# Kernel tuning notes

Measured on AMD Instinct MI355X. Metric: run time of the kernel, lower is better.

Reference implementation:

```python
import jax, jax.numpy as jnp
import numpy as np

jax.config.update("jax_enable_x64", True)

B, N, M_EQ, D_INEQ = 64, 128, 32, 64
RHO = 1.0
THRES = 1e-5
MAX_ITERS = 5000  # safety cap (original loops until relative objective change <= 1e-5)


def setup_inputs() -> dict:
    key = jax.random.key(0)
    kL, kq, kG, kA, kx0, ks = jax.random.split(key, 6)
    L = jax.random.normal(kL, (B, N, N))
    Q = jnp.einsum('bij,bkj->bik', L, L) / N + jnp.eye(N)  # SPD, well-conditioned
    q = jax.random.normal(kq, (B, N))
    G = jax.random.normal(kG, (B, D_INEQ, N))
    A = jax.random.normal(kA, (B, M_EQ, N))
    x0 = jax.random.normal(kx0, (B, N))
    slack = jax.random.uniform(ks, (B, D_INEQ)) + 0.1
    h = jnp.einsum('bdn,bn->bd', G, x0) + slack  # strictly feasible ineq
    b = jnp.einsum('bmn,bn->bm', A, x0)          # feasible eq
    f32 = jnp.float32
    return {"Q": Q.astype(f32), "q": q.astype(f32), "G": G.astype(f32),
            "h": h.astype(f32), "A": A.astype(f32), "b": b.astype(f32)}


def _alt_diff_batch(Q, q, G, h, A, b):
    """Batched Alt-Diff ADMM QP solve; returns (x [B,n], dx/dq [B,n,n])."""
    Bb, n = q.shape
    d = h.shape[1]
    m = b.shape[1]
    dt = Q.dtype
    AtA = jnp.einsum('bmi,bmj->bij', A, A)
    GtG = jnp.einsum('bdi,bdj->bij', G, G)
    R = -jnp.linalg.inv(Q + RHO * AtA + RHO * GtG)
    ATb = RHO * jnp.einsum('bmn,bm->bn', A, b)
    GTh = RHO * jnp.einsum('bdn,bd->bn', G, h)
    eye = jnp.eye(n, dtype=dt)

    def obj(x):
        return 0.5 * jnp.einsum('bi,bij,bj->b', x, Q, x) + jnp.einsum('bi,bi->b', q, x)

    init = dict(
        xk=jnp.zeros((Bb, n), dt), sk=jnp.zeros((Bb, d), dt),
        lamb=jnp.zeros((Bb, m), dt), nu=jnp.zeros((Bb, d), dt),
        dxk=jnp.zeros((Bb, n, n), dt), dsk=jnp.zeros((Bb, d, n), dt),
        dlamb=jnp.zeros((Bb, m, n), dt), dnu=jnp.zeros((Bb, d, n), dt),
        res_prev=jnp.full((Bb,), 1000.0, dt),   # res = [1000, -100] init
        res_cur=jnp.full((Bb,), -100.0, dt),
        done=jnp.zeros((Bb,), bool),
        it=jnp.zeros((), jnp.int32),
    )

    def cond(s):
        return jnp.logical_and(jnp.any(~s["done"]), s["it"] < MAX_ITERS)

    def body(s):
        xk = jnp.einsum('bij,bj->bi', R,
                        q + jnp.einsum('bmn,bm->bn', A, s["lamb"])
                          + jnp.einsum('bdn,bd->bn', G, s["nu"]) - ATb
                          + RHO * jnp.einsum('bdn,bd->bn', G, s["sk"]) - GTh)
        dxk = jnp.einsum('bij,bjk->bik', R,
                         eye + jnp.einsum('bmn,bmk->bnk', A, s["dlamb"])
                             + jnp.einsum('bdn,bdk->bnk', G, s["dnu"])
                             + RHO * jnp.einsum('bdn,bdk->bnk', G, s["dsk"]))
        Gx = jnp.einsum('bdn,bn->bd', G, xk)
        sk = jax.nn.relu(-(1.0 / RHO) * s["nu"] - (Gx - h))
        sgn = (sk > 0).astype(dt)  # sgn applied to already-relu'd sk, as in source
        dsk = (-1.0 / RHO) * sgn[:, :, None] * (s["dnu"] + RHO * jnp.einsum('bdn,bnk->bdk', G, dxk))
        lamb = s["lamb"] + RHO * (jnp.einsum('bmn,bn->bm', A, xk) - b)
        dlamb = s["dlamb"] + RHO * jnp.einsum('bmn,bnk->bmk', A, dxk)
        nu = s["nu"] + RHO * (Gx + sk - h)
        dnu = s["dnu"] + RHO * (jnp.einsum('bdn,bnk->bdk', G, dxk) + dsk)
        res_new = obj(xk)

        keep = s["done"]

        def sel(old, new):
            mask = keep.reshape((-1,) + (1,) * (new.ndim - 1))
            return jnp.where(mask, old, new)

        res_prev = jnp.where(keep, s["res_prev"], s["res_cur"])
        res_cur = jnp.where(keep, s["res_cur"], res_new)
        done = keep | (jnp.abs((res_cur - res_prev) / res_prev) <= THRES)
        return dict(
            xk=sel(s["xk"], xk), sk=sel(s["sk"], sk),
            lamb=sel(s["lamb"], lamb), nu=sel(s["nu"], nu),
            dxk=sel(s["dxk"], dxk), dsk=sel(s["dsk"], dsk),
            dlamb=sel(s["dlamb"], dlamb), dnu=sel(s["dnu"], dnu),
            res_prev=res_prev, res_cur=res_cur, done=done, it=s["it"] + 1,
        )

    final = jax.lax.while_loop(cond, body, init)
    return final["xk"], final["dxk"]


def reference(Q, q, G, h, A, b):
    out_dtype = q.dtype
    f64 = jnp.float64
    x, _dx = _alt_diff_batch(Q.astype(f64), q.astype(f64), G.astype(f64),
                             h.astype(f64), A.astype(f64), b.astype(f64))
    return x.astype(out_dtype)
```

## Files before the change

### kernel.cpp

```cpp
#include <hip/hip_runtime.h>

#define NN 128
#define ME 32
#define DI 64
#define NZ 96
#define ROWD 130
#define MAXIT 5000

#define OFF_UN 16640
#define ROWB  (OFF_UN)
#define COLB  (OFF_UN + 256)
#define PPK   (OFF_UN)
#define ZEXL  (OFF_UN + 256)
#define ZEXH  (OFF_UN + 384)
#define TVX   (OFF_UN + 448)
#define TV16  (OFF_UN + 576)
#define FLG   (OFF_UN + 608)
#define YBUF  (OFF_UN)
#define KBUF  (OFF_UN + 1536)
#define CPART (OFF_UN + 1024)
#define VP    (OFF_UN + 1280)
#define BASEV (OFF_UN + 1792)
#define QBV   (OFF_UN + 1888)
#define FPART (OFF_UN + 1024)
#define RHSV  (OFF_UN + 1280)
#define XPART (OFF_UN + 1408)
#define CB    (OFF_UN + 2688)
#define QBUF  (OFF_UN + 2816)
#define V1    (OFF_UN + 2944)
#define V2    (OFF_UN + 3072)
#define HB    (OFF_UN + 3200)
#define BB    (OFF_UN + 3264)
#define CST   (OFF_UN + 3296)
#define ZBF   (OFF_UN + 3304)
#define LDS_DBL (OFF_UN + 3400)

typedef __attribute__((ext_vector_type(2))) float f32x2;

__device__ __forceinline__ float rlf(float v, int lane) {
  return __uint_as_float((unsigned)__builtin_amdgcn_readlane((int)__float_as_uint(v), lane));
}
__device__ __forceinline__ f32x2 fma2(f32x2 a, f32x2 b, f32x2 c) {
  return __builtin_elementwise_fma(a, b, c);
}

#define MV2(PA, ZS, L0) {                                                  \
    f32x2 z0 = { rlf(ZS, L0), rlf(ZS, (L0)+1) };                           \
    A0 = fma2(Kp[PA], z0, A0); B0 = fma2(Kp2[PA], z0, B0);                 \
    f32x2 z1 = { rlf(ZS, (L0)+2), rlf(ZS, (L0)+3) };                       \
    A1 = fma2(Kp[(PA)+1], z1, A1); B1 = fma2(Kp2[(PA)+1], z1, B1); }

#define CPY12(LB)                                                          \
  _Pragma("unroll") for (int p = 0; p < 6; ++p) {                          \
    Kp [(LB)+p].x = (float)ldsd[KBUF + (2*p  )*NZ + l];                    \
    Kp [(LB)+p].y = (float)ldsd[KBUF + (2*p+1)*NZ + l];                    \
    Kp2[(LB)+p].x = (float)ldsd[KBUF + (2*p  )*NZ + 64 + lm];              \
    Kp2[(LB)+p].y = (float)ldsd[KBUF + (2*p+1)*NZ + 64 + lm];              \
  }

__global__ __launch_bounds__(256, 1) void altdiff_kernel(
    const float* __restrict__ Qg, const float* __restrict__ qg,
    const float* __restrict__ Gg, const float* __restrict__ hg,
    const float* __restrict__ Ag, const float* __restrict__ bg,
    float* __restrict__ out)
{
  extern __shared__ double ldsd[];

  const int bidx = blockIdx.x;
  const int tid  = threadIdx.x;
  const int w    = tid >> 6;
  const int l    = tid & 63;
  const int lm   = l & 31;
  const int ia   = tid & 127;
  const int hh   = tid >> 7;

  const float* Qb = Qg + (size_t)bidx * NN * NN;
  const float* Ab = Ag + (size_t)bidx * ME * NN;
  const float* Gb = Gg + (size_t)bidx * DI * NN;
  const float* qb = qg + (size_t)bidx * NN;
  const float* hb = hg + (size_t)bidx * DI;
  const float* bv = bg + (size_t)bidx * ME;

  if (tid < DI) ldsd[HB + tid] = (double)hb[tid];
  else if (tid < DI + ME) ldsd[BB + tid - DI] = (double)bv[tid - DI];
  if (tid >= 128) ldsd[QBUF + tid - 128] = (double)qb[tid - 128];

  const int r = tid >> 4, c = tid & 15;
  double acc[8][8];

  {
    const float4* Q4 = (const float4*)Qb;
#pragma unroll
    for (int rr = 0; rr < 8; ++rr) {
      float4 q0 = Q4[((8*r+rr) << 5) + 2*c];
      float4 q1 = Q4[((8*r+rr) << 5) + 2*c + 1];
      acc[rr][0]=(double)q0.x; acc[rr][1]=(double)q0.y; acc[rr][2]=(double)q0.z; acc[rr][3]=(double)q0.w;
      acc[rr][4]=(double)q1.x; acc[rr][5]=(double)q1.y; acc[rr][6]=(double)q1.z; acc[rr][7]=(double)q1.w;
    }
    const float4* A4 = (const float4*)Ab;
    for (int m = 0; m < ME; ++m) {
      float4 u0 = A4[(m << 5) + 2*r], u1 = A4[(m << 5) + 2*r + 1];
      float4 v0 = A4[(m << 5) + 2*c], v1 = A4[(m << 5) + 2*c + 1];
      double uu[8] = {(double)u0.x,(double)u0.y,(double)u0.z,(double)u0.w,
                      (double)u1.x,(double)u1.y,(double)u1.z,(double)u1.w};
      double vv[8] = {(double)v0.x,(double)v0.y,(double)v0.z,(double)v0.w,
                      (double)v1.x,(double)v1.y,(double)v1.z,(double)v1.w};
#pragma unroll
      for (int rr = 0; rr < 8; ++rr)
#pragma unroll
        for (int cc = 0; cc < 8; ++cc)
          acc[rr][cc] = fma(uu[rr], vv[cc], acc[rr][cc]);
    }
    const float4* G4 = (const float4*)Gb;
    for (int d = 0; d < DI; ++d) {
      float4 u0 = G4[(d << 5) + 2*r], u1 = G4[(d << 5) + 2*r + 1];
      float4 v0 = G4[(d << 5) + 2*c], v1 = G4[(d << 5) + 2*c + 1];
      double uu[8] = {(double)u0.x,(double)u0.y,(double)u0.z,(double)u0.w,
                      (double)u1.x,(double)u1.y,(double)u1.z,(double)u1.w};
      double vv[8] = {(double)v0.x,(double)v0.y,(double)v0.z,(double)v0.w,
                      (double)v1.x,(double)v1.y,(double)v1.z,(double)v1.w};
#pragma unroll
      for (int rr = 0; rr < 8; ++rr)
#pragma unroll
        for (int cc = 0; cc < 8; ++cc)
          acc[rr][cc] = fma(uu[rr], vv[cc], acc[rr][cc]);
    }
  }

  {
    if (r == 0) {
#pragma unroll
      for (int cc = 0; cc < 8; ++cc) ldsd[ROWB + 8*c + cc] = acc[0][cc];
    }
    if (c == 0) {
#pragma unroll
      for (int rr = 0; rr < 8; ++rr) ldsd[COLB + 8*r + rr] = acc[rr][0];
    }
    __syncthreads();
    for (int k = 0; k < NN; ++k) {
      const int pb = (k & 1) << 7;
      const int krt = k >> 3, kcl = k & 7;
      double rowk[8], colv[8];
#pragma unroll
      for (int cc = 0; cc < 8; ++cc) rowk[cc] = ldsd[ROWB + pb + 8*c + cc];
#pragma unroll
      for (int rr = 0; rr < 8; ++rr) colv[rr] = ldsd[COLB + pb + 8*r + rr];
      const double dkk  = ldsd[ROWB + pb + k];
      const double rcpd = 1.0 / dkk;
      double rdv[8];
#pragma unroll
      for (int cc = 0; cc < 8; ++cc) rdv[cc] = rowk[cc] * rcpd;
      const bool pivR = (r == krt), pivC = (c == krt);
#pragma unroll
      for (int rr = 0; rr < 8; ++rr) {
        const double cv = colv[rr] * rcpd;
        const bool pr = pivR && (rr == kcl);
#pragma unroll
        for (int cc = 0; cc < 8; ++cc) {
          double gen = fma(-cv, rowk[cc], acc[rr][cc]);
          acc[rr][cc] = pr ? rdv[cc] : gen;
        }
      }
      if (pivC) {
#pragma unroll
        for (int cc = 0; cc < 8; ++cc) if (cc == kcl) {
#pragma unroll
          for (int rr = 0; rr < 8; ++rr) {
            const bool pr2 = pivR && (rr == kcl);
            acc[rr][cc] = pr2 ? -rcpd : colv[rr] * rcpd;
          }
        }
      }
      if (k < NN - 1) {
        const int pb2 = ((k + 1) & 1) << 7;
        const int krt2 = (k + 1) >> 3, kcl2 = (k + 1) & 7;
        if (r == krt2) {
#pragma unroll
          for (int rr = 0; rr < 8; ++rr) if (rr == kcl2) {
#pragma unroll
            for (int cc = 0; cc < 8; ++cc) ldsd[ROWB + pb2 + 8*c + cc] = acc[rr][cc];
          }
        }
        if (c == krt2) {
#pragma unroll
          for (int cc = 0; cc < 8; ++cc) if (cc == kcl2) {
#pragma unroll
            for (int rr = 0; rr < 8; ++rr) ldsd[COLB + pb2 + 8*r + rr] = acc[rr][cc];
          }
        }
      }
      __syncthreads();
    }
#pragma unroll
    for (int rr = 0; rr < 8; ++rr) {
      double2* dst = (double2*)(ldsd + (8*r+rr)*ROWD + 8*c);
#pragma unroll
      for (int t = 0; t < 4; ++t) dst[t] = make_double2(acc[rr][2*t], acc[rr][2*t+1]);
    }
  }
  __syncthreads();

  f32x2 Kp[24], Kp2[24];
  for (int blk = 0; blk < 8; ++blk) {
    {
      const float* gp[6];
#pragma unroll
      for (int jj = 0; jj < 6; ++jj) {
        int it = 12*blk + 6*hh + jj;
        gp[jj] = (it < DI) ? (Gb + it*NN) : (Ab + (it - DI)*NN);
      }
      double a2[6] = {0,0,0,0,0,0};
#pragma unroll 4
      for (int t = 0; t < NN; ++t) {
        double rv = ldsd[t*ROWD + ia];
#pragma unroll
        for (int jj = 0; jj < 6; ++jj)
          a2[jj] = fma(rv, (double)gp[jj][t], a2[jj]);
      }
      double2* yst = (double2*)(ldsd + YBUF + ia*12 + 6*hh);
#pragma unroll
      for (int p = 0; p < 3; ++p) yst[p] = make_double2(a2[2*p], a2[2*p+1]);
    }
    __syncthreads();
    {
      const int r2 = (ia < NZ) ? ia : 0;
      const float* brow = (r2 < DI) ? (Gb + r2*NN) : (Ab + (r2 - DI)*NN);
      double a2[6] = {0,0,0,0,0,0};
#pragma unroll 4
      for (int t = 0; t < NN; ++t) {
        double bvv = (double)brow[t];
        const double2* yr = (const double2*)(ldsd + YBUF + t*12 + 6*hh);
        double2 y0 = yr[0], y1 = yr[1], y2 = yr[2];
        a2[0] = fma(bvv, y0.x, a2[0]); a2[1] = fma(bvv, y0.y, a2[1]);
        a2[2] = fma(bvv, y1.x, a2[2]); a2[3] = fma(bvv, y1.y, a2[3]);
        a2[4] = fma(bvv, y2.x, a2[4]); a2[5] = fma(bvv, y2.y, a2[5]);
      }
      if (ia < NZ) {
#pragma unroll
        for (int jj = 0; jj < 6; ++jj) ldsd[KBUF + (6*hh + jj)*NZ + ia] = a2[jj];
      }
    }
    __syncthreads();
    if (w == 0) {
      if (blk == 0)      { CPY12(0) }
      else if (blk == 1) { CPY12(6) }
      else if (blk == 2) { CPY12(12) }
      else if (blk == 3) { CPY12(18) }
    } else if (w == 1) {
      if (blk == 4)      { CPY12(0) }
      else if (blk == 5) { CPY12(6) }
      else if (blk == 6) { CPY12(12) }
      else if (blk == 7) { CPY12(18) }
    }
    __syncthreads();
  }

  {
    double s = 0;
#pragma unroll 8
    for (int jc = 0; jc < 48; ++jc) {
      int j = 48*hh + jc;
      double coef = (j < DI) ? ldsd[HB + j] : ldsd[BB + j - DI];
      const float* src = (j < DI) ? (Gb + j*NN) : (Ab + (j - DI)*NN);
      s = fma(-(double)src[ia], coef, s);
    }
    ldsd[CPART + hh*128 + ia] = s;
  }
  __syncthreads();
  if (tid < NN) ldsd[CB + tid] = ldsd[QBUF + tid] + ldsd[CPART + tid] + ldsd[CPART + 128 + tid];
  __syncthreads();

  {
    double a = 0, b2 = 0;
#pragma unroll 4
    for (int tt = 0; tt < 64; ++tt) {
      int t = 64*hh + tt;
      double rv = ldsd[t*ROWD + ia];
      a  = fma(rv, ldsd[CB + t], a);
      b2 = fma(rv, ldsd[QBUF + t], b2);
    }
    ldsd[VP + hh*128 + ia] = a;
    ldsd[VP + 256 + hh*128 + ia] = b2;
  }
  __syncthreads();
  if (tid < NN) {
    ldsd[V1 + tid] = ldsd[VP + tid] + ldsd[VP + 128 + tid];
    ldsd[V2 + tid] = ldsd[VP + 256 + tid] + ldsd[VP + 384 + tid];
  }
  __syncthreads();

  {
    const int r2 = (ia < NZ) ? ia : 0;
    const float* brow = (r2 < DI) ? (Gb + r2*NN) : (Ab + (r2 - DI)*NN);
    const int voff = hh ? V2 : V1;
    double s = 0;
#pragma unroll 4
    for (int t = 0; t < NN; ++t) s = fma((double)brow[t], ldsd[voff + t], s);
    if (ia < NZ) ldsd[(hh ? QBV : BASEV) + ia] = s;
  }
  if (w == 0) {
    double pc = ldsd[V1+l]*ldsd[CB+l]   + ldsd[V1+64+l]*ldsd[CB+64+l];
    double pq = ldsd[V1+l]*ldsd[QBUF+l] + ldsd[V1+64+l]*ldsd[QBUF+64+l];
#pragma unroll
    for (int off = 32; off >= 1; off >>= 1) { pc += __shfl_xor(pc, off); pq += __shfl_xor(pq, off); }
    if (l == 0) { ldsd[CST] = pc; ldsd[CST+1] = pq; }
  }
  __syncthreads();

  const double baseA = ldsd[BASEV + l];
  const double baseB = ldsd[BASEV + 64 + lm];
  const double qvA   = ldsd[QBV + l];
  const double qvB   = ldsd[QBV + 64 + lm];
  const double hb2   = ldsd[HB + l] - baseA;
  const double bb2   = baseB - ldsd[BB + lm];
  const double S_uc  = ldsd[CST], S_qu = ldsd[CST + 1];
  double hnb = hb2, lb = bb2;
  double zlo = 0.0, zhi = 0.0;
  double zAlo = 0.0, zAhi = 0.0, zBlo = 0.0, zBhi = 0.0, zClo = 0.0, zChi = 0.0;
  double res_prev = 1000.0, res_cur = -100.0;
  float2 own = make_float2(0.f, 0.f);

  {
    if (w < 2) *(float2*)&ldsd[PPK + w*64 + l] = make_float2(0.f, 0.f);
    if (w == 0) ldsd[ZEXL + 64 + l] = 0.0;
    if (w == 1 && l < 32) ldsd[ZEXH + 32 + l] = 0.0;
    if (tid == 0) { ldsd[FLG] = 0.0; ldsd[FLG + 1] = 0.0; }
  }

  for (int it = 0; it < MAXIT + 3; ++it) {
    __syncthreads();
    const int buf = it & 1, nbuf = buf ^ 1;
    const int bprev = nbuf;
    const double fl = ldsd[FLG + bprev];

    if (w < 2) {
      float2 rem = *(const float2*)&ldsd[PPK + buf*128 + (w ^ 1)*64 + l];
      float slo = own.x + rem.x;
      double t = hnb - (double)slo;
      float zflo = (float)fabs(t);
      float zfhi = 0.f;
      double lamn = 0.0;
      if (w == 1) {
        float shi = own.y + rem.y;
        lamn = lb + (double)shi;
        zfhi = (float)lamn;
      }
      if (it >= 3 && fl != 0.0) break;
      if (w == 0) { zClo = zBlo; zBlo = zAlo; zAlo = zlo; }
      else        { zChi = zBhi; zBhi = zAhi; zAhi = zhi; }
      if (it < MAXIT) {
        if (w == 0) { zlo = fabs(t); ldsd[ZEXL + buf*64 + l] = zlo; }
        hnb = hb2 + fmin(t, 0.0);
        if (w == 1) {
          zhi = lamn; lb = lamn + bb2;
          if (l < 32) ldsd[ZEXH + buf*32 + l] = lamn;
        }
        f32x2 A0 = {0.f, 0.f}, A1 = A0, B0 = A0, B1 = A0;
        if (w == 0) {
          MV2(0,  zflo, 0)  MV2(2,  zflo, 4)  MV2(4,  zflo, 8)  MV2(6,  zflo, 12)
          MV2(8,  zflo, 16) MV2(10, zflo, 20) MV2(12, zflo, 24) MV2(14, zflo, 28)
          MV2(16, zflo, 32) MV2(18, zflo, 36) MV2(20, zflo, 40) MV2(22, zflo, 44)
        } else {
          MV2(0,  zflo, 48) MV2(2,  zflo, 52) MV2(4,  zflo, 56) MV2(6,  zflo, 60)
          MV2(8,  zfhi, 0)  MV2(10, zfhi, 4)  MV2(12, zfhi, 8)  MV2(14, zfhi, 12)
          MV2(16, zfhi, 16) MV2(18, zfhi, 20) MV2(20, zfhi, 24) MV2(22, zfhi, 28)
        }
        f32x2 As = A0 + A1, Bs = B0 + B1;
        float2 np = make_float2(As.x + As.y, Bs.x + Bs.y);
        *(float2*)&ldsd[PPK + nbuf*128 + w*64 + l] = np;
        own = np;
      }
    } else if (w == 2) {
      const float2* pb = (const float2*)(ldsd + PPK + buf*128);
      float2 v0 = pb[l], v1 = pb[64 + l];
      const double zAl = ldsd[ZEXL + bprev*64 + l];
      const double zAh = ldsd[ZEXH + bprev*32 + lm];
      const int g = l & 15;
      const double* tq = ldsd + TVX + bprev*64;
      double a0 = tq[g], a1 = tq[g + 16], a2 = tq[g + 32], a3 = tq[g + 48];
      if (it >= 3 && fl != 0.0) break;
      if (it < MAXIT) {
        float slo_f = v0.x + v1.x;
        float shi_f = v0.y + v1.y;
        double yf  = (double)slo_f + baseA;
        double tvl = fma(qvA, zAl, -0.5*(zAl*(baseA + yf) + yf*yf));
        double yfB = (double)shi_f + baseB;
        double tvh = fma(qvB, zAh, -0.5*(zAh*(baseB + yfB) + yfB*yfB));
        ldsd[TVX + buf*64 + l] = tvl + ((l < 32) ? tvh : 0.0);
      }
      if (l < 16 && it >= 1 && it <= MAXIT)
        ldsd[TV16 + buf*16 + l] = (a0 + a1) + (a2 + a3);
    } else {
      double t1v[16];
      const double2* tp = (const double2*)(ldsd + TV16 + bprev*16);
#pragma unroll
      for (int u = 0; u < 8; ++u) { double2 vv = tp[u]; t1v[2*u] = vv.x; t1v[2*u+1] = vv.y; }
      if (it >= 3 && fl != 0.0) break;
      if (it >= 2 && it <= MAXIT + 1) {
        double s1 = ((t1v[0] + t1v[1]) + (t1v[2] + t1v[3])) + ((t1v[4] + t1v[5]) + (t1v[6] + t1v[7]));
        double s2 = ((t1v[8] + t1v[9]) + (t1v[10] + t1v[11])) + ((t1v[12] + t1v[13]) + (t1v[14] + t1v[15]));
        double obj = (s1 + s2) - 0.5*S_uc + S_qu;
        res_prev = res_cur; res_cur = obj;
        if (l == 0)
          ldsd[FLG + buf] = (fabs(res_cur - res_prev) <= 1e-5 * fabs(res_prev)) ? 1.0 : 0.0;
      }
    }
  }

  if (w == 0) ldsd[ZBF + l] = zClo;
  if (w == 1 && l < 32) ldsd[ZBF + 64 + l] = zChi;
  __syncthreads();
  {
    double s = 0;
#pragma unroll 8
    for (int jc = 0; jc < 48; ++jc) {
      int j = 48*hh + jc;
      double zj = ldsd[ZBF + j];
      const float* src = (j < DI) ? (Gb + j*NN) : (Ab + (j - DI)*NN);
      s = fma((double)src[ia], zj, s);
    }
    ldsd[FPART + hh*128 + ia] = s;
  }
  __syncthreads();
  if (tid < NN) ldsd[RHSV + tid] = ldsd[CB + tid] + ldsd[FPART + tid] + ldsd[FPART + 128 + tid];
  __syncthreads();
  {
    double s = 0;
#pragma unroll 4
    for (int tt = 0; tt < 64; ++tt) {
      int t = 64*hh + tt;
      s = fma(ldsd[t*ROWD + ia], ldsd[RHSV + t], s);
    }
    ldsd[XPART + hh*128 + ia] = s;
  }
  __syncthreads();
  if (tid < NN)
    out[(size_t)bidx * NN + tid] = (float)(ldsd[XPART + tid] + ldsd[XPART + 128 + tid]);
}

extern "C" void kernel_launch(void* const* d_in, const int* in_sizes, int n_in,
                              void* d_out, int out_size, void* d_ws, size_t ws_size,
                              hipStream_t stream) {
  (void)in_sizes; (void)n_in; (void)out_size; (void)d_ws; (void)ws_size;
  const float* Q = (const float*)d_in[0];
  const float* q = (const float*)d_in[1];
  const float* G = (const float*)d_in[2];
  const float* h = (const float*)d_in[3];
  const float* A = (const float*)d_in[4];
  const float* b = (const float*)d_in[5];
  float* out = (float*)d_out;
  const size_t lds_bytes = (size_t)LDS_DBL * sizeof(double);
  altdiff_kernel<<<dim3(64), dim3(256), lds_bytes, stream>>>(Q, q, G, h, A, b, out);
}
```

Before: 631.0 us.

## Split iteration matvec across three wavefronts instead of two

The per-iteration 96x96 matvec over the z vector, previously split across two wavefronts with 48 columns each, is now spread over three wavefronts with 32 columns each. The objective-evaluation and convergence-check wavefronts are merged into one. The aim is to shorten the critical path of each serial ADMM iteration, since each wave does fewer readlane+FMA steps. In exchange, each iteration reads three partial-sum buffers instead of two, and the last wave carries more serial work.

```diff
diff --git a/kernel.cpp b/kernel.cpp
--- a/kernel.cpp
+++ b/kernel.cpp
@@ -11,11 +11,11 @@
 #define ROWB  (OFF_UN)
 #define COLB  (OFF_UN + 256)
 #define PPK   (OFF_UN)
-#define ZEXL  (OFF_UN + 256)
-#define ZEXH  (OFF_UN + 384)
-#define TVX   (OFF_UN + 448)
-#define TV16  (OFF_UN + 576)
-#define FLG   (OFF_UN + 608)
+#define ZEXL  (OFF_UN + 384)
+#define ZEXH  (OFF_UN + 512)
+#define TVX   (OFF_UN + 576)
+#define TV16  (OFF_UN + 704)
+#define FLG   (OFF_UN + 736)
 #define YBUF  (OFF_UN)
 #define KBUF  (OFF_UN + 1536)
 #define CPART (OFF_UN + 1024)
@@ -50,12 +50,13 @@
     f32x2 z1 = { rlf(ZS, (L0)+2), rlf(ZS, (L0)+3) };                       \
     A1 = fma2(Kp[(PA)+1], z1, A1); B1 = fma2(Kp2[(PA)+1], z1, B1); }
 
-#define CPY12(LB)                                                          \
-  _Pragma("unroll") for (int p = 0; p < 6; ++p) {                          \
-    Kp [(LB)+p].x = (float)ldsd[KBUF + (2*p  )*NZ + l];                    \
-    Kp [(LB)+p].y = (float)ldsd[KBUF + (2*p+1)*NZ + l];                    \
-    Kp2[(LB)+p].x = (float)ldsd[KBUF + (2*p  )*NZ + 64 + lm];              \
-    Kp2[(LB)+p].y = (float)ldsd[KBUF + (2*p+1)*NZ + 64 + lm];              \
+#define CPYRANGE(LBASE, KBASE, CNT)                                        \
+  _Pragma("unroll") for (int j = 0; j < (CNT); ++j) {                      \
+    const int lj = (LBASE) + j, kc = (KBASE) + j;                          \
+    float va = (float)ldsd[KBUF + kc*NZ + l];                              \
+    float vb = (float)ldsd[KBUF + kc*NZ + 64 + lm];                        \
+    if ((lj & 1) == 0) { Kp[lj>>1].x = va; Kp2[lj>>1].x = vb; }            \
+    else               { Kp[lj>>1].y = va; Kp2[lj>>1].y = vb; }            \
   }
 
 __global__ __launch_bounds__(256, 1) void altdiff_kernel(
@@ -200,7 +201,7 @@
   }
   __syncthreads();
 
-  f32x2 Kp[24], Kp2[24];
+  f32x2 Kp[16], Kp2[16];
   for (int blk = 0; blk < 8; ++blk) {
     {
       const float* gp[6];
@@ -242,15 +243,18 @@
     }
     __syncthreads();
     if (w == 0) {
-      if (blk == 0)      { CPY12(0) }
-      else if (blk == 1) { CPY12(6) }
-      else if (blk == 2) { CPY12(12) }
-      else if (blk == 3) { CPY12(18) }
+      if (blk == 0)      { CPYRANGE(0,  0, 12) }
+      else if (blk == 1) { CPYRANGE(12, 0, 12) }
+      else if (blk == 2) { CPYRANGE(24, 0, 8) }
     } else if (w == 1) {
-      if (blk == 4)      { CPY12(0) }
-      else if (blk == 5) { CPY12(6) }
-      else if (blk == 6) { CPY12(12) }
-      else if (blk == 7) { CPY12(18) }
+      if (blk == 2)      { CPYRANGE(0,  8, 4) }
+      else if (blk == 3) { CPYRANGE(4,  0, 12) }
+      else if (blk == 4) { CPYRANGE(16, 0, 12) }
+      else if (blk == 5) { CPYRANGE(28, 0, 4) }
+    } else if (w == 2) {
+      if (blk == 5)      { CPYRANGE(0,  4, 8) }
+      else if (blk == 6) { CPYRANGE(8,  0, 12) }
+      else if (blk == 7) { CPYRANGE(20, 0, 12) }
     }
     __syncthreads();
   }
@@ -321,9 +325,9 @@
   float2 own = make_float2(0.f, 0.f);
 
   {
-    if (w < 2) *(float2*)&ldsd[PPK + w*64 + l] = make_float2(0.f, 0.f);
+    if (w < 3) *(float2*)&ldsd[PPK + w*64 + l] = make_float2(0.f, 0.f);
     if (w == 0) ldsd[ZEXL + 64 + l] = 0.0;
-    if (w == 1 && l < 32) ldsd[ZEXH + 32 + l] = 0.0;
+    if (w == 2 && l < 32) ldsd[ZEXH + 32 + l] = 0.0;
     if (tid == 0) { ldsd[FLG] = 0.0; ldsd[FLG + 1] = 0.0; }
   }
 
@@ -332,56 +336,77 @@
     const int buf = it & 1, nbuf = buf ^ 1;
     const int bprev = nbuf;
     const double fl = ldsd[FLG + bprev];
-
-    if (w < 2) {
-      float2 rem = *(const float2*)&ldsd[PPK + buf*128 + (w ^ 1)*64 + l];
-      float slo = own.x + rem.x;
+    const float2* pb = (const float2*)(ldsd + PPK + buf*192);
+
+    if (w == 0) {
+      float2 s1v = pb[64 + l], s2v = pb[128 + l];
+      float slo = (own.x + s1v.x) + s2v.x;
       double t = hnb - (double)slo;
       float zflo = (float)fabs(t);
-      float zfhi = 0.f;
-      double lamn = 0.0;
-      if (w == 1) {
-        float shi = own.y + rem.y;
-        lamn = lb + (double)shi;
-        zfhi = (float)lamn;
-      }
       if (it >= 3 && fl != 0.0) break;
-      if (w == 0) { zClo = zBlo; zBlo = zAlo; zAlo = zlo; }
-      else        { zChi = zBhi; zBhi = zAhi; zAhi = zhi; }
+      zClo = zBlo; zBlo = zAlo; zAlo = zlo;
       if (it < MAXIT) {
-        if (w == 0) { zlo = fabs(t); ldsd[ZEXL + buf*64 + l] = zlo; }
+        zlo = fabs(t);
+        ldsd[ZEXL + buf*64 + l] = zlo;
         hnb = hb2 + fmin(t, 0.0);
-        if (w == 1) {
-          zhi = lamn; lb = lamn + bb2;
-          if (l < 32) ldsd[ZEXH + buf*32 + l] = lamn;
-        }
         f32x2 A0 = {0.f, 0.f}, A1 = A0, B0 = A0, B1 = A0;
-        if (w == 0) {
-          MV2(0,  zflo, 0)  MV2(2,  zflo, 4)  MV2(4,  zflo, 8)  MV2(6,  zflo, 12)
-          MV2(8,  zflo, 16) MV2(10, zflo, 20) MV2(12, zflo, 24) MV2(14, zflo, 28)
-          MV2(16, zflo, 32) MV2(18, zflo, 36) MV2(20, zflo, 40) MV2(22, zflo, 44)
-        } else {
-          MV2(0,  zflo, 48) MV2(2,  zflo, 52) MV2(4,  zflo, 56) MV2(6,  zflo, 60)
-          MV2(8,  zfhi, 0)  MV2(10, zfhi, 4)  MV2(12, zfhi, 8)  MV2(14, zfhi, 12)
-          MV2(16, zfhi, 16) MV2(18, zfhi, 20) MV2(20, zfhi, 24) MV2(22, zfhi, 28)
-        }
+        MV2(0,  zflo, 0)  MV2(2,  zflo, 4)  MV2(4,  zflo, 8)  MV2(6,  zflo, 12)
+        MV2(8,  zflo, 16) MV2(10, zflo, 20) MV2(12, zflo, 24) MV2(14, zflo, 28)
         f32x2 As = A0 + A1, Bs = B0 + B1;
         float2 np = make_float2(As.x + As.y, Bs.x + Bs.y);
-        *(float2*)&ldsd[PPK + nbuf*128 + w*64 + l] = np;
+        *(float2*)&ldsd[PPK + nbuf*192 + l] = np;
         own = np;
       }
+    } else if (w == 1) {
+      float2 s0v = pb[l], s2v = pb[128 + l];
+      float slo = (s0v.x + own.x) + s2v.x;
+      double t = hnb - (double)slo;
+      float zflo = (float)fabs(t);
+      if (it >= 3 && fl != 0.0) break;
+      if (it < MAXIT) {
+        hnb = hb2 + fmin(t, 0.0);
+        f32x2 A0 = {0.f, 0.f}, A1 = A0, B0 = A0, B1 = A0;
+        MV2(0,  zflo, 32) MV2(2,  zflo, 36) MV2(4,  zflo, 40) MV2(6,  zflo, 44)
+        MV2(8,  zflo, 48) MV2(10, zflo, 52) MV2(12, zflo, 56) MV2(14, zflo, 60)
+        f32x2 As = A0 + A1, Bs = B0 + B1;
+        float2 np = make_float2(As.x + As.y, Bs.x + Bs.y);
+        *(float2*)&ldsd[PPK + nbuf*192 + 64 + l] = np;
+        own = np;
+      }
     } else if (w == 2) {
-      const float2* pb = (const float2*)(ldsd + PPK + buf*128);
-      float2 v0 = pb[l], v1 = pb[64 + l];
+      float2 s0v = pb[l], s1v = pb[64 + l];
+      float shi = (s0v.y + s1v.y) + own.y;
+      double lamn = lb + (double)shi;
+      float zfhi = (float)lamn;
+      if (it >= 3 && fl != 0.0) break;
+      zChi = zBhi; zBhi = zAhi; zAhi = zhi;
+      if (it < MAXIT) {
+        zhi = lamn;
+        lb = lamn + bb2;
+        if (l < 32) ldsd[ZEXH + buf*32 + l] = lamn;
+        f32x2 A0 = {0.f, 0.f}, A1 = A0, B0 = A0, B1 = A0;
+        MV2(0,  zfhi, 0)  MV2(2,  zfhi, 4)  MV2(4,  zfhi, 8)  MV2(6,  zfhi, 12)
+        MV2(8,  zfhi, 16) MV2(10, zfhi, 20) MV2(12, zfhi, 24) MV2(14, zfhi, 28)
+        f32x2 As = A0 + A1, Bs = B0 + B1;
+        float2 np = make_float2(As.x + As.y, Bs.x + Bs.y);
+        *(float2*)&ldsd[PPK + nbuf*192 + 128 + l] = np;
+        own = np;
+      }
+    } else {
+      float2 v0 = pb[l], v1 = pb[64 + l], v2 = pb[128 + l];
       const double zAl = ldsd[ZEXL + bprev*64 + l];
       const double zAh = ldsd[ZEXH + bprev*32 + lm];
       const int g = l & 15;
       const double* tq = ldsd + TVX + bprev*64;
       double a0 = tq[g], a1 = tq[g + 16], a2 = tq[g + 32], a3 = tq[g + 48];
+      double t1v[16];
+      const double2* tp = (const double2*)(ldsd + TV16 + bprev*16);
+#pragma unroll
+      for (int u = 0; u < 8; ++u) { double2 vv = tp[u]; t1v[2*u] = vv.x; t1v[2*u+1] = vv.y; }
       if (it >= 3 && fl != 0.0) break;
       if (it < MAXIT) {
-        float slo_f = v0.x + v1.x;
-        float shi_f = v0.y + v1.y;
+        float slo_f = (v0.x + v1.x) + v2.x;
+        float shi_f = (v0.y + v1.y) + v2.y;
         double yf  = (double)slo_f + baseA;
         double tvl = fma(qvA, zAl, -0.5*(zAl*(baseA + yf) + yf*yf));
         double yfB = (double)shi_f + baseB;
@@ -390,12 +415,6 @@
       }
       if (l < 16 && it >= 1 && it <= MAXIT)
         ldsd[TV16 + buf*16 + l] = (a0 + a1) + (a2 + a3);
-    } else {
-      double t1v[16];
-      const double2* tp = (const double2*)(ldsd + TV16 + bprev*16);
-#pragma unroll
-      for (int u = 0; u < 8; ++u) { double2 vv = tp[u]; t1v[2*u] = vv.x; t1v[2*u+1] = vv.y; }
-      if (it >= 3 && fl != 0.0) break;
       if (it >= 2 && it <= MAXIT + 1) {
         double s1 = ((t1v[0] + t1v[1]) + (t1v[2] + t1v[3])) + ((t1v[4] + t1v[5]) + (t1v[6] + t1v[7]));
         double s2 = ((t1v[8] + t1v[9]) + (t1v[10] + t1v[11])) + ((t1v[12] + t1v[13]) + (t1v[14] + t1v[15]));
@@ -408,7 +427,7 @@
   }
 
   if (w == 0) ldsd[ZBF + l] = zClo;
-  if (w == 1 && l < 32) ldsd[ZBF + 64 + l] = zChi;
+  if (w == 2 && l < 32) ldsd[ZBF + 64 + l] = zChi;
   __syncthreads();
   {
     double s = 0;
```

New measurement: 598.7 us (median of 2 runs). -5.1%, faster.

## Split ADMM matvec across all four waves instead of two

Applied to the files above, without the earlier changes.

Spreads the per-iteration 96-wide matvec over four wavefronts, each holding 12 register-resident K columns instead of 24, and has every wave read all four partial-sum buffers from LDS. The objective-term work moves onto wave 2 and the TV16 reduction onto wave 1, so the separate ZEXL/ZEXH exchange buffers go away. The z history is now kept in float rather than double. This should shorten the serial critical path of each iteration and ease register pressure, at the cost of more LDS reads per wave and slightly lower precision in the stored z values.

```diff
diff --git a/kernel.cpp b/kernel.cpp
--- a/kernel.cpp
+++ b/kernel.cpp
@@ -11,11 +11,9 @@
 #define ROWB  (OFF_UN)
 #define COLB  (OFF_UN + 256)
 #define PPK   (OFF_UN)
-#define ZEXL  (OFF_UN + 256)
-#define ZEXH  (OFF_UN + 384)
-#define TVX   (OFF_UN + 448)
-#define TV16  (OFF_UN + 576)
-#define FLG   (OFF_UN + 608)
+#define TVX   (OFF_UN + 512)
+#define TV16  (OFF_UN + 640)
+#define FLG   (OFF_UN + 672)
 #define YBUF  (OFF_UN)
 #define KBUF  (OFF_UN + 1536)
 #define CPART (OFF_UN + 1024)
@@ -200,7 +198,7 @@
   }
   __syncthreads();
 
-  f32x2 Kp[24], Kp2[24];
+  f32x2 Kp[12], Kp2[12];
   for (int blk = 0; blk < 8; ++blk) {
     {
       const float* gp[6];
@@ -241,16 +239,8 @@
       }
     }
     __syncthreads();
-    if (w == 0) {
-      if (blk == 0)      { CPY12(0) }
-      else if (blk == 1) { CPY12(6) }
-      else if (blk == 2) { CPY12(12) }
-      else if (blk == 3) { CPY12(18) }
-    } else if (w == 1) {
-      if (blk == 4)      { CPY12(0) }
-      else if (blk == 5) { CPY12(6) }
-      else if (blk == 6) { CPY12(12) }
-      else if (blk == 7) { CPY12(18) }
+    if (w == (blk >> 1)) {
+      if ((blk & 1) == 0) { CPY12(0) } else { CPY12(6) }
     }
     __syncthreads();
   }
@@ -315,15 +305,15 @@
   const double bb2   = baseB - ldsd[BB + lm];
   const double S_uc  = ldsd[CST], S_qu = ldsd[CST + 1];
   double hnb = hb2, lb = bb2;
-  double zlo = 0.0, zhi = 0.0;
-  double zAlo = 0.0, zAhi = 0.0, zBlo = 0.0, zBhi = 0.0, zClo = 0.0, zChi = 0.0;
+  float hnbf = (float)hnb, lbf = (float)lb;
+  float zpl = 0.f, zph = 0.f;
+  float zpl2 = 0.f, zph2 = 0.f;
+  float zAf_lo = 0.f, zBf_lo = 0.f, zCf_lo = 0.f;
+  float zAf_hi = 0.f, zBf_hi = 0.f, zCf_hi = 0.f;
   double res_prev = 1000.0, res_cur = -100.0;
-  float2 own = make_float2(0.f, 0.f);
-
-  {
-    if (w < 2) *(float2*)&ldsd[PPK + w*64 + l] = make_float2(0.f, 0.f);
-    if (w == 0) ldsd[ZEXL + 64 + l] = 0.0;
-    if (w == 1 && l < 32) ldsd[ZEXH + 32 + l] = 0.0;
+
+  {
+    *(float2*)&ldsd[PPK + w*64 + l] = make_float2(0.f, 0.f);
     if (tid == 0) { ldsd[FLG] = 0.0; ldsd[FLG + 1] = 0.0; }
   }
 
@@ -332,70 +322,82 @@
     const int buf = it & 1, nbuf = buf ^ 1;
     const int bprev = nbuf;
     const double fl = ldsd[FLG + bprev];
-
-    if (w < 2) {
-      float2 rem = *(const float2*)&ldsd[PPK + buf*128 + (w ^ 1)*64 + l];
-      float slo = own.x + rem.x;
-      double t = hnb - (double)slo;
-      float zflo = (float)fabs(t);
-      float zfhi = 0.f;
-      double lamn = 0.0;
-      if (w == 1) {
-        float shi = own.y + rem.y;
-        lamn = lb + (double)shi;
-        zfhi = (float)lamn;
-      }
+    const float2* pb = (const float2*)(ldsd + PPK + buf*256);
+    float2 p0 = pb[l], p1 = pb[64 + l], p2 = pb[128 + l], p3 = pb[192 + l];
+
+    if (w == 0) {
+      float slo = (p0.x + p1.x) + (p2.x + p3.x);
+      float zflo = fabsf(hnbf - slo);
       if (it >= 3 && fl != 0.0) break;
-      if (w == 0) { zClo = zBlo; zBlo = zAlo; zAlo = zlo; }
-      else        { zChi = zBhi; zBhi = zAhi; zAhi = zhi; }
+      zCf_lo = zBf_lo; zBf_lo = zAf_lo; zAf_lo = zpl;
       if (it < MAXIT) {
-        if (w == 0) { zlo = fabs(t); ldsd[ZEXL + buf*64 + l] = zlo; }
-        hnb = hb2 + fmin(t, 0.0);
-        if (w == 1) {
-          zhi = lamn; lb = lamn + bb2;
-          if (l < 32) ldsd[ZEXH + buf*32 + l] = lamn;
-        }
-        f32x2 A0 = {0.f, 0.f}, A1 = A0, B0 = A0, B1 = A0;
-        if (w == 0) {
-          MV2(0,  zflo, 0)  MV2(2,  zflo, 4)  MV2(4,  zflo, 8)  MV2(6,  zflo, 12)
-          MV2(8,  zflo, 16) MV2(10, zflo, 20) MV2(12, zflo, 24) MV2(14, zflo, 28)
-          MV2(16, zflo, 32) MV2(18, zflo, 36) MV2(20, zflo, 40) MV2(22, zflo, 44)
-        } else {
-          MV2(0,  zflo, 48) MV2(2,  zflo, 52) MV2(4,  zflo, 56) MV2(6,  zflo, 60)
-          MV2(8,  zfhi, 0)  MV2(10, zfhi, 4)  MV2(12, zfhi, 8)  MV2(14, zfhi, 12)
-          MV2(16, zfhi, 16) MV2(18, zfhi, 20) MV2(20, zfhi, 24) MV2(22, zfhi, 28)
-        }
+        zpl = zflo;
+        double t = hnb - (double)slo; hnb = hb2 + fmin(t, 0.0); hnbf = (float)hnb;
+        f32x2 A0 = {0.f,0.f}, A1 = A0, B0 = A0, B1 = A0;
+        MV2(0,  zflo, 0)  MV2(2,  zflo, 4)  MV2(4,  zflo, 8)
+        MV2(6,  zflo, 12) MV2(8,  zflo, 16) MV2(10, zflo, 20)
         f32x2 As = A0 + A1, Bs = B0 + B1;
-        float2 np = make_float2(As.x + As.y, Bs.x + Bs.y);
-        *(float2*)&ldsd[PPK + nbuf*128 + w*64 + l] = np;
-        own = np;
-      }
-    } else if (w == 2) {
-      const float2* pb = (const float2*)(ldsd + PPK + buf*128);
-      float2 v0 = pb[l], v1 = pb[64 + l];
-      const double zAl = ldsd[ZEXL + bprev*64 + l];
-      const double zAh = ldsd[ZEXH + bprev*32 + lm];
+        *(float2*)&ldsd[PPK + nbuf*256 + l] = make_float2(As.x + As.y, Bs.x + Bs.y);
+      }
+    } else if (w == 1) {
       const int g = l & 15;
       const double* tq = ldsd + TVX + bprev*64;
       double a0 = tq[g], a1 = tq[g + 16], a2 = tq[g + 32], a3 = tq[g + 48];
+      float slo = (p0.x + p1.x) + (p2.x + p3.x);
+      float zflo = fabsf(hnbf - slo);
       if (it >= 3 && fl != 0.0) break;
       if (it < MAXIT) {
-        float slo_f = v0.x + v1.x;
-        float shi_f = v0.y + v1.y;
-        double yf  = (double)slo_f + baseA;
+        double t = hnb - (double)slo; hnb = hb2 + fmin(t, 0.0); hnbf = (float)hnb;
+        f32x2 A0 = {0.f,0.f}, A1 = A0, B0 = A0, B1 = A0;
+        MV2(0,  zflo, 24) MV2(2,  zflo, 28) MV2(4,  zflo, 32)
+        MV2(6,  zflo, 36) MV2(8,  zflo, 40) MV2(10, zflo, 44)
+        f32x2 As = A0 + A1, Bs = B0 + B1;
+        *(float2*)&ldsd[PPK + nbuf*256 + 64 + l] = make_float2(As.x + As.y, Bs.x + Bs.y);
+      }
+      if (l < 16 && it >= 1 && it <= MAXIT)
+        ldsd[TV16 + buf*16 + l] = (a0 + a1) + (a2 + a3);
+    } else if (w == 2) {
+      float slo = (p0.x + p1.x) + (p2.x + p3.x);
+      float shi = (p0.y + p1.y) + (p2.y + p3.y);
+      float zflo = fabsf(hnbf - slo);
+      float zfhi = lbf + shi;
+      if (it >= 3 && fl != 0.0) break;
+      const float zAl_f = zpl2, zAh_f = zph2;
+      if (it < MAXIT) {
+        zpl2 = zflo; zph2 = zfhi;
+        double t = hnb - (double)slo; hnb = hb2 + fmin(t, 0.0); hnbf = (float)hnb;
+        double lamn = lb + (double)shi; lb = lamn + bb2; lbf = (float)lb;
+        f32x2 A0 = {0.f,0.f}, A1 = A0, B0 = A0, B1 = A0;
+        MV2(0,  zflo, 48) MV2(2,  zflo, 52) MV2(4,  zflo, 56) MV2(6,  zflo, 60)
+        MV2(8,  zfhi, 0)  MV2(10, zfhi, 4)
+        f32x2 As = A0 + A1, Bs = B0 + B1;
+        *(float2*)&ldsd[PPK + nbuf*256 + 128 + l] = make_float2(As.x + As.y, Bs.x + Bs.y);
+        double zAl = (double)zAl_f;
+        double yf  = (double)slo + baseA;
         double tvl = fma(qvA, zAl, -0.5*(zAl*(baseA + yf) + yf*yf));
-        double yfB = (double)shi_f + baseB;
+        double zAh = (double)zAh_f;
+        double yfB = (double)shi + baseB;
         double tvh = fma(qvB, zAh, -0.5*(zAh*(baseB + yfB) + yfB*yfB));
         ldsd[TVX + buf*64 + l] = tvl + ((l < 32) ? tvh : 0.0);
       }
-      if (l < 16 && it >= 1 && it <= MAXIT)
-        ldsd[TV16 + buf*16 + l] = (a0 + a1) + (a2 + a3);
     } else {
       double t1v[16];
       const double2* tp = (const double2*)(ldsd + TV16 + bprev*16);
 #pragma unroll
       for (int u = 0; u < 8; ++u) { double2 vv = tp[u]; t1v[2*u] = vv.x; t1v[2*u+1] = vv.y; }
+      float shi = (p0.y + p1.y) + (p2.y + p3.y);
+      float zfhi = lbf + shi;
       if (it >= 3 && fl != 0.0) break;
+      zCf_hi = zBf_hi; zBf_hi = zAf_hi; zAf_hi = zph;
+      if (it < MAXIT) {
+        zph = zfhi;
+        double lamn = lb + (double)shi; lb = lamn + bb2; lbf = (float)lb;
+        f32x2 A0 = {0.f,0.f}, A1 = A0, B0 = A0, B1 = A0;
+        MV2(0,  zfhi, 8)  MV2(2,  zfhi, 12) MV2(4,  zfhi, 16)
+        MV2(6,  zfhi, 20) MV2(8,  zfhi, 24) MV2(10, zfhi, 28)
+        f32x2 As = A0 + A1, Bs = B0 + B1;
+        *(float2*)&ldsd[PPK + nbuf*256 + 192 + l] = make_float2(As.x + As.y, Bs.x + Bs.y);
+      }
       if (it >= 2 && it <= MAXIT + 1) {
         double s1 = ((t1v[0] + t1v[1]) + (t1v[2] + t1v[3])) + ((t1v[4] + t1v[5]) + (t1v[6] + t1v[7]));
         double s2 = ((t1v[8] + t1v[9]) + (t1v[10] + t1v[11])) + ((t1v[12] + t1v[13]) + (t1v[14] + t1v[15]));
@@ -407,8 +409,8 @@
     }
   }
 
-  if (w == 0) ldsd[ZBF + l] = zClo;
-  if (w == 1 && l < 32) ldsd[ZBF + 64 + l] = zChi;
+  if (w == 0) ldsd[ZBF + l] = (double)zCf_lo;
+  if (w == 3 && l < 32) ldsd[ZBF + 64 + l] = (double)zCf_hi;
   __syncthreads();
   {
     double s = 0;
```

Result: slower. 653.1 us (+3.5%).
